# Kernel optimization log

Hardware: AMD Instinct MI355X
Metric: run time of the kernel (lower is better)

Reference implementation:

```python
import math
import jax, jax.numpy as jnp
import numpy as np

NEG_INF = -jnp.inf


def setup_inputs() -> dict:
    key = jax.random.key(0)
    k1, k2, k3 = jax.random.split(key, 3)
    B, T, D = 2, 2048, 1024
    x = jax.random.normal(k1, (B, T, D), dtype=jnp.float32)
    w_qkv = jax.random.normal(k2, (3 * D, D), dtype=jnp.float32) * (1.0 / math.sqrt(D))
    w_out = jax.random.normal(k3, (D, D), dtype=jnp.float32) * (1.0 / math.sqrt(D))
    return {"x": x, "w_qkv": w_qkv, "w_out": w_out, "n_heads": 16, "k": 8}


def reference(x, w_qkv, w_out, n_heads, k):
    B, T, D = x.shape
    head_dim = D // n_heads
    scale = math.sqrt(head_dim)

    qkv = x @ w_qkv.T                                   # (B,T,3D), torch Linear: x W^T
    q, kk, v = jnp.split(qkv, 3, axis=-1)

    def split_heads(t):
        return t.reshape(B, T, n_heads, head_dim).transpose(0, 2, 1, 3)  # (B,H,T,dh)

    q, kk, v = split_heads(q), split_heads(kk), split_heads(v)

    scores = jnp.einsum("bhqd,bhkd->bhqk", q, kk) / scale  # (B,H,T,T)
    causal = jnp.tril(jnp.ones((T, T), dtype=bool))
    scores = jnp.where(causal, scores, NEG_INF)

    # per-row effective k: min(k, n_valid) with n_valid = row index + 1
    top_vals = jax.lax.top_k(scores, k)[0]                 # (B,H,T,k), sorted desc
    k_eff_idx = jnp.minimum(jnp.arange(1, T + 1), k) - 1   # (T,)
    thresh = jnp.take_along_axis(
        top_vals, k_eff_idx[None, None, :, None], axis=-1  # (B,H,T,1)
    )
    keep = scores >= thresh                                # ties kept, matching torch >=
    scores = jnp.where(keep, scores, NEG_INF)

    attn = jax.nn.softmax(scores, axis=-1)
    attn = jnp.nan_to_num(attn)                            # defensive; rows never all -inf
    out = jnp.einsum("bhqk,bhkd->bhqd", attn, v)
    out = out.transpose(0, 2, 1, 3).reshape(B, T, D)       # merge heads
    return out @ w_out.T
```

## Files before the change

kernel.cpp:

```cpp
#include <hip/hip_runtime.h>
#include <hip/hip_bf16.h>
#include <math.h>
#include <float.h>

#define NUM_B 2
#define SEQ_T 2048
#define DIM_D 1024
#define NH 16
#define DH 64
#define KDIM 1024
#define KSEL 8

#define CAP 32
#define MFMA_MARGIN 0.06f

typedef __attribute__((ext_vector_type(8))) short bf16x8v;
typedef __attribute__((ext_vector_type(4))) float f32x4v;
typedef __attribute__((ext_vector_type(4))) double f64x4v;

__device__ __forceinline__ float bf2f(unsigned int u) {
  union { unsigned int i; float f; } v; v.i = u << 16; return v.f;
}

__device__ __forceinline__ short f2bs(float f) {
  __hip_bfloat16 h = __float2bfloat16(f);
  return *(short*)&h;
}

__device__ __forceinline__ void split8(float4 x0, float4 x1,
                                       unsigned short* __restrict__ hp,
                                       unsigned short* __restrict__ lp) {
  unsigned short h[8], l[8];
  const float xs[8] = {x0.x, x0.y, x0.z, x0.w, x1.x, x1.y, x1.z, x1.w};
#pragma unroll
  for (int j = 0; j < 8; ++j) {
    const short hb = f2bs(xs[j]);
    h[j] = (unsigned short)hb;
    const float hf = bf2f((unsigned int)(unsigned short)hb);
    l[j] = (unsigned short)f2bs(xs[j] - hf);
  }
  *(uint4*)hp = *(const uint4*)h;
  *(uint4*)lp = *(const uint4*)l;
}

__device__ __forceinline__ void split4(float4 x,
                                       unsigned short* __restrict__ hp,
                                       unsigned short* __restrict__ lp) {
  unsigned short h[4], l[4];
  const float xs[4] = {x.x, x.y, x.z, x.w};
#pragma unroll
  for (int j = 0; j < 4; ++j) {
    const short hb = f2bs(xs[j]);
    h[j] = (unsigned short)hb;
    const float hf = bf2f((unsigned int)(unsigned short)hb);
    l[j] = (unsigned short)f2bs(xs[j] - hf);
  }
  *(uint2*)hp = *(const uint2*)h;
  *(uint2*)lp = *(const uint2*)l;
}

__global__ __launch_bounds__(512) void gemm_qk(
    const float* __restrict__ A, const float* __restrict__ Bm,
    float* __restrict__ qbuf, float* __restrict__ kbuf,
    unsigned short* __restrict__ kbf) {
  __shared__ __align__(16) float As[64][36];
  __shared__ __align__(16) float Bs[128][36];
  const int tid = threadIdx.x;
  const int lane = tid & 63;
  const int w = tid >> 6;
  const int row0 = blockIdx.y * 64;
  const int col0 = blockIdx.x * 128;
  const int lrA = tid >> 3;
  const int lkA = (tid & 7) << 2;
  const int lrB = tid >> 2;
  const int lkB = (tid & 3) << 3;
  const float* ap = A + (size_t)(row0 + lrA) * KDIM + lkA;
  const float* bp = Bm + (size_t)(col0 + lrB) * KDIM + lkB;
  const int wr = (w >> 2) << 5;
  const int wc = (w & 3) << 5;
  const int li = lane & 15;
  const int lk4 = lane >> 4;

  int rowof[4], colof[4];
  {
    f64x4v pr = {0.0, 0.0, 0.0, 0.0};
    f64x4v pc = {0.0, 0.0, 0.0, 0.0};
    const double vidx = (double)li;
    pr = __builtin_amdgcn_mfma_f64_16x16x4f64(vidx, 1.0, pr, 0, 0, 0);
    pc = __builtin_amdgcn_mfma_f64_16x16x4f64(1.0, vidx, pc, 0, 0, 0);
#pragma unroll
    for (int vj = 0; vj < 4; ++vj) {
      rowof[vj] = (int)(pr[vj] * 0.25 + 0.5);
      colof[vj] = (int)(pc[vj] * 0.25 + 0.5);
    }
  }

  f64x4v acc[2][2];
#pragma unroll
  for (int m = 0; m < 2; ++m)
#pragma unroll
    for (int n = 0; n < 2; ++n)
      acc[m][n] = (f64x4v){0.0, 0.0, 0.0, 0.0};

  float4 ra = *(const float4*)(ap);
  float4 rb0 = *(const float4*)(bp);
  float4 rb1 = *(const float4*)(bp + 4);
  for (int k0 = 0; k0 < KDIM; k0 += 32) {
    __syncthreads();
    *(float4*)&As[lrA][lkA] = ra;
    *(float4*)&Bs[lrB][lkB] = rb0;
    *(float4*)&Bs[lrB][lkB + 4] = rb1;
    if (k0 + 32 < KDIM) {
      ra = *(const float4*)(ap + k0 + 32);
      rb0 = *(const float4*)(bp + k0 + 32);
      rb1 = *(const float4*)(bp + k0 + 36);
    }
    __syncthreads();
#pragma unroll
    for (int ks = 0; ks < 32; ks += 4) {
      const int kk = ks + lk4;
      const double af0 = (double)As[wr + li][kk];
      const double af1 = (double)As[wr + 16 + li][kk];
      const double bf0 = (double)Bs[wc + li][kk];
      const double bf1 = (double)Bs[wc + 16 + li][kk];
      acc[0][0] = __builtin_amdgcn_mfma_f64_16x16x4f64(af0, bf0, acc[0][0], 0, 0, 0);
      acc[0][1] = __builtin_amdgcn_mfma_f64_16x16x4f64(af0, bf1, acc[0][1], 0, 0, 0);
      acc[1][0] = __builtin_amdgcn_mfma_f64_16x16x4f64(af1, bf0, acc[1][0], 0, 0, 0);
      acc[1][1] = __builtin_amdgcn_mfma_f64_16x16x4f64(af1, bf1, acc[1][1], 0, 0, 0);
    }
  }

  const int bb = row0 >> 11;
  const int t0 = row0 & 2047;
#pragma unroll
  for (int m = 0; m < 2; ++m)
#pragma unroll
    for (int n = 0; n < 2; ++n)
#pragma unroll
      for (int vj = 0; vj < 4; ++vj) {
        const int r = wr + 16 * m + rowof[vj];
        const int gc = col0 + wc + 16 * n + colof[vj];
        const int qi = gc >> 10;
        const int head = (gc & 1023) >> 6;
        const int d = gc & 63;
        const int t = t0 + r;
        const float fv = (float)acc[m][n][vj];
        float* dst = ((qi == 0) ? qbuf : kbuf) +
                     (size_t)(bb * NH + head) * SEQ_T * DH;
        dst[(size_t)t * DH + d] = fv;
        if (qi == 1) {
          unsigned short* kb = kbf + ((size_t)(bb * NH + head) << 17);
          const int key = t & 127;
          const int off =
              (((t >> 7) << 13) | (key << 6) | d) ^ ((key & 7) << 3);
          __hip_bfloat16 hb = __float2bfloat16(fv);
          kb[off] = *(unsigned short*)&hb;
        }
      }
}

__global__ __launch_bounds__(512) void gemm_v(
    const float* __restrict__ A, const float* __restrict__ Bm,
    unsigned short* __restrict__ vbuf) {
  __shared__ __align__(16) unsigned short Ah[64][40];
  __shared__ __align__(16) unsigned short Al[64][40];
  __shared__ __align__(16) unsigned short Bh[128][40];
  __shared__ __align__(16) unsigned short Bl[128][40];
  const int tid = threadIdx.x;
  const int lane = tid & 63;
  const int w = tid >> 6;
  const int row0 = blockIdx.y * 64;
  const int col0v = blockIdx.x * 128;
  const int lrA = tid >> 3;
  const int lkA = (tid & 7) << 2;
  const int lrB = tid >> 2;
  const int lkB = (tid & 3) << 3;
  const float* ap = A + (size_t)(row0 + lrA) * KDIM + lkA;
  const float* bp = Bm + (size_t)(col0v + lrB) * KDIM + lkB;
  const int wr = (w >> 2) << 5;
  const int wc = (w & 3) << 5;
  const int li = lane & 15;
  const int kA = (lane >> 4) << 3;

  f32x4v acc[2][2];
#pragma unroll
  for (int m = 0; m < 2; ++m)
#pragma unroll
    for (int n = 0; n < 2; ++n)
      acc[m][n] = (f32x4v){0.f, 0.f, 0.f, 0.f};

  float4 ra = *(const float4*)(ap);
  float4 rb0 = *(const float4*)(bp);
  float4 rb1 = *(const float4*)(bp + 4);
  for (int k0 = 0; k0 < KDIM; k0 += 32) {
    __syncthreads();
    split4(ra, &Ah[lrA][lkA], &Al[lrA][lkA]);
    split8(rb0, rb1, &Bh[lrB][lkB], &Bl[lrB][lkB]);
    if (k0 + 32 < KDIM) {
      ra = *(const float4*)(ap + k0 + 32);
      rb0 = *(const float4*)(bp + k0 + 32);
      rb1 = *(const float4*)(bp + k0 + 36);
    }
    __syncthreads();
    bf16x8v ah[2], al[2], bh[2], bl[2];
#pragma unroll
    for (int m = 0; m < 2; ++m) {
      ah[m] = *(const bf16x8v*)&Ah[wr + 16 * m + li][kA];
      al[m] = *(const bf16x8v*)&Al[wr + 16 * m + li][kA];
      bh[m] = *(const bf16x8v*)&Bh[wc + 16 * m + li][kA];
      bl[m] = *(const bf16x8v*)&Bl[wc + 16 * m + li][kA];
    }
#pragma unroll
    for (int m = 0; m < 2; ++m)
#pragma unroll
      for (int n = 0; n < 2; ++n) {
        acc[m][n] = __builtin_amdgcn_mfma_f32_16x16x32_bf16(ah[m], bh[n], acc[m][n], 0, 0, 0);
        acc[m][n] = __builtin_amdgcn_mfma_f32_16x16x32_bf16(ah[m], bl[n], acc[m][n], 0, 0, 0);
        acc[m][n] = __builtin_amdgcn_mfma_f32_16x16x32_bf16(al[m], bh[n], acc[m][n], 0, 0, 0);
      }
  }

  const int bb = row0 >> 11;
  const int t0 = row0 & 2047;
  const int r4 = (lane >> 4) << 2;
#pragma unroll
  for (int m = 0; m < 2; ++m)
#pragma unroll
    for (int n = 0; n < 2; ++n)
#pragma unroll
      for (int j = 0; j < 4; ++j) {
        const int t = t0 + wr + 16 * m + r4 + j;
        const int vcol = col0v + wc + 16 * n + li;
        const int head = vcol >> 6;
        const int d = vcol & 63;
        vbuf[(size_t)(bb * NH + head) * SEQ_T * DH + (size_t)t * DH + d] =
            (unsigned short)f2bs(acc[m][n][j]);
      }
}

__global__ __launch_bounds__(512) void attn_topk(
    const float* __restrict__ q, const float* __restrict__ kmat,
    const unsigned short* __restrict__ kbf,
    const unsigned short* __restrict__ v, unsigned short* __restrict__ ctx) {
  __shared__ __align__(16) unsigned short kt[128 * 64];
  __shared__ double cs64[128][CAP];
  __shared__ short ckey[128][CAP];
  __shared__ int ccnt[128];
  __shared__ double rthr[128];
  __shared__ float rmx[128];

  const int tid = threadIdx.x;
  const int lane = tid & 63;
  const int w = tid >> 6;
  const int bh = blockIdx.x & 31;
  const int u = blockIdx.x >> 5;
  const int g = (u < 8) ? u : 23 - u;
  const int t0 = g << 7;
  const size_t kbase = (size_t)bh * SEQ_T * DH;
  const int wrow0 = t0 + (w << 4);
  const int kA = (lane >> 4) << 3;
  const int rbase = wrow0 + ((lane >> 4) << 2);

  bf16x8v qa0, qa1;
  {
    const float* qr = q + kbase + (size_t)(wrow0 + (lane & 15)) * DH;
    const float4 x0 = *(const float4*)(qr + kA);
    const float4 x1 = *(const float4*)(qr + kA + 4);
    const float4 y0 = *(const float4*)(qr + 32 + kA);
    const float4 y1 = *(const float4*)(qr + 32 + kA + 4);
    qa0[0] = f2bs(x0.x); qa0[1] = f2bs(x0.y);
    qa0[2] = f2bs(x0.z); qa0[3] = f2bs(x0.w);
    qa0[4] = f2bs(x1.x); qa0[5] = f2bs(x1.y);
    qa0[6] = f2bs(x1.z); qa0[7] = f2bs(x1.w);
    qa1[0] = f2bs(y0.x); qa1[1] = f2bs(y0.y);
    qa1[2] = f2bs(y0.z); qa1[3] = f2bs(y0.w);
    qa1[4] = f2bs(y1.x); qa1[5] = f2bs(y1.y);
    qa1[6] = f2bs(y1.z); qa1[7] = f2bs(y1.w);
  }

  const uint4* ksrc = (const uint4*)(kbf + ((size_t)bh << 17));
  const int nt = (t0 >> 7) + 1;
  const int wmax = wrow0 + 15;

  float tq[4][8];
#pragma unroll
  for (int j = 0; j < 4; ++j)
#pragma unroll
    for (int m = 0; m < 8; ++m) tq[j][m] = -FLT_MAX;

  for (int T = 0; T < nt; ++T) {
    if (T) __syncthreads();
    {
      const uint4* st = ksrc + (size_t)T * 1024;
      uint4* dv = (uint4*)kt;
#pragma unroll
      for (int i = 0; i < 2; ++i) dv[i * 512 + tid] = st[i * 512 + tid];
    }
    __syncthreads();
    const int glim0 = (wmax - (T << 7)) >> 4;
    const int glim = glim0 > 7 ? 7 : glim0;
    for (int gt = 0; gt <= glim; ++gt) {
      const int kk = (gt << 4) + (lane & 15);
      const int key = (T << 7) + kk;
      const int b0 = ((kk << 7) | (kA << 1)) ^ ((kk & 7) << 4);
      const int b1 = ((kk << 7) | ((32 + kA) << 1)) ^ ((kk & 7) << 4);
      const bf16x8v kb0 = *(const bf16x8v*)((const char*)kt + b0);
      const bf16x8v kb1 = *(const bf16x8v*)((const char*)kt + b1);
      f32x4v acc = {0.f, 0.f, 0.f, 0.f};
      acc = __builtin_amdgcn_mfma_f32_16x16x32_bf16(qa0, kb0, acc, 0, 0, 0);
      acc = __builtin_amdgcn_mfma_f32_16x16x32_bf16(qa1, kb1, acc, 0, 0, 0);
#pragma unroll
      for (int j = 0; j < 4; ++j) {
        float sc = acc[j] * 0.125f;
        sc = (key <= rbase + j) ? sc : -FLT_MAX;
        if (sc > tq[j][7]) {
          float s = sc;
#pragma unroll
          for (int m = 0; m < 8; ++m) {
            const float hi = fmaxf(tq[j][m], s);
            s = fminf(tq[j][m], s);
            tq[j][m] = hi;
          }
        }
      }
    }
  }

#pragma unroll
  for (int j = 0; j < 4; ++j) {
#pragma unroll
    for (int xm = 1; xm < 16; xm <<= 1) {
      float m[8];
#pragma unroll
      for (int i = 0; i < 8; ++i) {
        const float pb = __shfl_xor(tq[j][7 - i], xm);
        m[i] = fmaxf(tq[j][i], pb);
      }
#pragma unroll
      for (int d = 4; d >= 1; d >>= 1)
#pragma unroll
        for (int i = 0; i < 8; ++i)
          if ((i & d) == 0 && (i | d) < 8) {
            const float hi = fmaxf(m[i], m[i | d]);
            const float lo = fminf(m[i], m[i | d]);
            m[i] = hi;
            m[i | d] = lo;
          }
#pragma unroll
      for (int i = 0; i < 8; ++i) tq[j][i] = m[i];
    }
  }
  float thrj[4];
#pragma unroll
  for (int j = 0; j < 4; ++j) {
    const int kf = (rbase + j + 1 < KSEL) ? (rbase + j + 1) : KSEL;
    float th = tq[j][7];
#pragma unroll
    for (int m = 0; m < 8; ++m)
      if (m == kf - 1) th = tq[j][m];
    thrj[j] = th - MFMA_MARGIN;
  }

  if (tid < 128) ccnt[tid] = 0;
  __syncthreads();

  for (int T = 0; T < nt; ++T) {
    if (T) __syncthreads();
    {
      const uint4* st = ksrc + (size_t)T * 1024;
      uint4* dv = (uint4*)kt;
#pragma unroll
      for (int i = 0; i < 2; ++i) dv[i * 512 + tid] = st[i * 512 + tid];
    }
    __syncthreads();
    const int glim0 = (wmax - (T << 7)) >> 4;
    const int glim = glim0 > 7 ? 7 : glim0;
    for (int gt = 0; gt <= glim; ++gt) {
      const int kk = (gt << 4) + (lane & 15);
      const int key = (T << 7) + kk;
      const int b0 = ((kk << 7) | (kA << 1)) ^ ((kk & 7) << 4);
      const int b1 = ((kk << 7) | ((32 + kA) << 1)) ^ ((kk & 7) << 4);
      const bf16x8v kb0 = *(const bf16x8v*)((const char*)kt + b0);
      const bf16x8v kb1 = *(const bf16x8v*)((const char*)kt + b1);
      f32x4v acc = {0.f, 0.f, 0.f, 0.f};
      acc = __builtin_amdgcn_mfma_f32_16x16x32_bf16(qa0, kb0, acc, 0, 0, 0);
      acc = __builtin_amdgcn_mfma_f32_16x16x32_bf16(qa1, kb1, acc, 0, 0, 0);
#pragma unroll
      for (int j = 0; j < 4; ++j) {
        const float sc = acc[j] * 0.125f;
        if (key <= rbase + j && sc >= thrj[j]) {
          const int rl = (w << 4) + ((lane >> 4) << 2) + j;
          const int p = atomicAdd(&ccnt[rl], 1);
          if (p < CAP) ckey[rl][p] = (short)key;
        }
      }
    }
  }

  const int lid = lane & 31;
  for (int rp = 0; rp < 8; ++rp) {
    const int rl = (w << 4) + (rp << 1) + (lane >> 5);
    const int ncc = ccnt[rl] < CAP ? ccnt[rl] : CAP;
    if (lid < ncc) {
      const int key = ckey[rl][lid];
      const float* qr = q + kbase + (size_t)(t0 + rl) * DH;
      const float* kr = kmat + kbase + (size_t)key * DH;
      double s = 0.0;
#pragma unroll
      for (int d4 = 0; d4 < 16; ++d4) {
        const float4 qq = *(const float4*)(qr + (d4 << 2));
        const float4 kq = *(const float4*)(kr + (d4 << 2));
        s = fma((double)qq.x, (double)kq.x, s);
        s = fma((double)qq.y, (double)kq.y, s);
        s = fma((double)qq.z, (double)kq.z, s);
        s = fma((double)qq.w, (double)kq.w, s);
      }
      cs64[rl][lid] = s * 0.125;
    }
  }
  __syncthreads();

  if (lane < 16) {
    const int rl = (w << 4) + lane;
    const int trow = t0 + rl;
    const int ncc = ccnt[rl] < CAP ? ccnt[rl] : CAP;
    double a64[8];
#pragma unroll
    for (int j = 0; j < 8; ++j) a64[j] = -DBL_MAX;
    for (int l = 0; l < ncc; ++l) {
      double sv = cs64[rl][l];
#pragma unroll
      for (int j = 0; j < 8; ++j) {
        const double hi = fmax(a64[j], sv);
        sv = fmin(a64[j], sv);
        a64[j] = hi;
      }
    }
    const int kf = (trow + 1 < KSEL) ? (trow + 1) : KSEL;
    double th = a64[7];
#pragma unroll
    for (int j = 0; j < 8; ++j)
      if (j == kf - 1) th = a64[j];
    rthr[rl] = th;
    rmx[rl] = (float)a64[0];
  }
  __syncthreads();

  for (int rg = 0; rg < 4; ++rg) {
    const int rlb = (w << 4) + (rg << 2);
    float acv[4] = {0.f, 0.f, 0.f, 0.f};
    float Zs[4] = {0.f, 0.f, 0.f, 0.f};
    int ncs[4];
    double ths[4];
    float mxs[4];
#pragma unroll
    for (int j = 0; j < 4; ++j) {
      const int rl = rlb + j;
      ncs[j] = ccnt[rl] < CAP ? ccnt[rl] : CAP;
      ths[j] = rthr[rl];
      mxs[j] = rmx[rl];
    }
    int nmax = ncs[0];
#pragma unroll
    for (int j = 1; j < 4; ++j) nmax = ncs[j] > nmax ? ncs[j] : nmax;
    for (int l = 0; l < nmax; ++l) {
#pragma unroll
      for (int j = 0; j < 4; ++j) {
        const int rl = rlb + j;
        if (l < ncs[j]) {
          const double s = cs64[rl][l];
          const float wgl = (s >= ths[j]) ? expf((float)s - mxs[j]) : 0.f;
          Zs[j] += wgl;
          acv[j] = fmaf(
              wgl,
              bf2f((unsigned int)v[kbase + (size_t)ckey[rl][l] * DH + lane]),
              acv[j]);
        }
      }
    }
#pragma unroll
    for (int j = 0; j < 4; ++j) {
      const int trow = t0 + rlb + j;
      __hip_bfloat16 h = __float2bfloat16(acv[j] / Zs[j]);
      ctx[((size_t)(bh >> 4) * SEQ_T + trow) * DIM_D + (bh & 15) * DH + lane] =
          *(unsigned short*)&h;
    }
  }
}

__global__ __launch_bounds__(256) void gemm_out(
    const unsigned short* __restrict__ A, const float* __restrict__ Bm,
    float* __restrict__ obuf) {
  __shared__ __align__(16) unsigned short Ah[64][40];
  __shared__ __align__(16) unsigned short Bh[64][40];
  __shared__ __align__(16) unsigned short Bl[64][40];
  const int tid = threadIdx.x;
  const int lane = tid & 63;
  const int w = tid >> 6;
  const int row0 = blockIdx.y * 64;
  const int col0 = blockIdx.x * 64;
  const int lrow = tid >> 2;
  const int lk = (tid & 3) << 3;
  const unsigned short* ap = A + (size_t)(row0 + lrow) * KDIM + lk;
  const float* bp = Bm + (size_t)(col0 + lrow) * KDIM + lk;
  const int wr = (w >> 1) << 5;
  const int wc = (w & 1) << 5;
  const int li = lane & 15;
  const int kA = (lane >> 4) << 3;

  f32x4v acc[2][2];
#pragma unroll
  for (int m = 0; m < 2; ++m)
#pragma unroll
    for (int n = 0; n < 2; ++n)
      acc[m][n] = (f32x4v){0.f, 0.f, 0.f, 0.f};

  uint4 ua = *(const uint4*)(ap);
  float4 rb0 = *(const float4*)(bp);
  float4 rb1 = *(const float4*)(bp + 4);
  for (int k0 = 0; k0 < KDIM; k0 += 32) {
    __syncthreads();
    *(uint4*)&Ah[lrow][lk] = ua;
    split8(rb0, rb1, &Bh[lrow][lk], &Bl[lrow][lk]);
    if (k0 + 32 < KDIM) {
      ua = *(const uint4*)(ap + k0 + 32);
      rb0 = *(const float4*)(bp + k0 + 32);
      rb1 = *(const float4*)(bp + k0 + 36);
    }
    __syncthreads();
    bf16x8v ah[2], bh[2], bl[2];
#pragma unroll
    for (int m = 0; m < 2; ++m) {
      ah[m] = *(const bf16x8v*)&Ah[wr + 16 * m + li][kA];
      bh[m] = *(const bf16x8v*)&Bh[wc + 16 * m + li][kA];
      bl[m] = *(const bf16x8v*)&Bl[wc + 16 * m + li][kA];
    }
#pragma unroll
    for (int m = 0; m < 2; ++m)
#pragma unroll
      for (int n = 0; n < 2; ++n) {
        acc[m][n] = __builtin_amdgcn_mfma_f32_16x16x32_bf16(ah[m], bh[n], acc[m][n], 0, 0, 0);
        acc[m][n] = __builtin_amdgcn_mfma_f32_16x16x32_bf16(ah[m], bl[n], acc[m][n], 0, 0, 0);
      }
  }

  const int r4 = (lane >> 4) << 2;
#pragma unroll
  for (int m = 0; m < 2; ++m)
#pragma unroll
    for (int n = 0; n < 2; ++n)
#pragma unroll
      for (int j = 0; j < 4; ++j) {
        const int r = row0 + wr + 16 * m + r4 + j;
        const int c = col0 + wc + 16 * n + li;
        obuf[(size_t)r * DIM_D + c] = acc[m][n][j];
      }
}

extern "C" void kernel_launch(void* const* d_in, const int* in_sizes, int n_in,
                              void* d_out, int out_size, void* d_ws,
                              size_t ws_size, hipStream_t stream) {
  (void)out_size; (void)ws_size;
  const float* x = (const float*)d_in[0];
  const float* wqkv = (const float*)d_in[1];
  const float* wout = (const float*)d_in[2];
  for (int i = 0; i < n_in; ++i) {
    if (in_sizes[i] == NUM_B * SEQ_T * DIM_D) x = (const float*)d_in[i];
    else if (in_sizes[i] == 3 * DIM_D * DIM_D) wqkv = (const float*)d_in[i];
    else if (in_sizes[i] == DIM_D * DIM_D) wout = (const float*)d_in[i];
  }
  float* out = (float*)d_out;

  const size_t qkv_elems = (size_t)NUM_B * NH * SEQ_T * DH;
  float* qbuf = (float*)d_ws;
  float* kbuf = qbuf + qkv_elems;
  unsigned short* vbuf = (unsigned short*)(kbuf + qkv_elems);
  unsigned short* ctxb = vbuf + qkv_elems;
  unsigned short* kbf = ctxb + (size_t)NUM_B * SEQ_T * DIM_D;

  gemm_qk<<<dim3(2 * DIM_D / 128, NUM_B * SEQ_T / 64), 512, 0, stream>>>(
      x, wqkv, qbuf, kbuf, kbf);
  gemm_v<<<dim3(DIM_D / 128, NUM_B * SEQ_T / 64), 512, 0, stream>>>(
      x, wqkv + (size_t)2 * DIM_D * KDIM, vbuf);
  attn_topk<<<dim3(NUM_B * NH * (SEQ_T / 128)), 512, 0, stream>>>(
      qbuf, kbuf, kbf, vbuf, ctxb);
  gemm_out<<<dim3(DIM_D / 64, NUM_B * SEQ_T / 64), 256, 0, stream>>>(
      ctxb, wout, out);
}
```

Before: 599.4 us.

## Split top-k attention into scan and selection kernels via global candidate buffer

The fused attention kernel is split in two. A scan kernel runs the MFMA score pass and writes per-row candidate keys and counts to workspace. A second kernel with 256 threads and 64-row tiles rescoring candidates in double precision, then does softmax and the V product. Moving the large double-precision shared arrays out of the scan kernel should cut its LDS footprint and raise occupancy, and the selection stage gets a finer grid. The cost is an extra launch plus a global round trip for the candidate lists, and the workspace layout must fit the new buffers.

```diff
diff --git a/kernel.cpp b/kernel.cpp
--- a/kernel.cpp
+++ b/kernel.cpp
@@ -238,16 +238,12 @@
       }
 }
 
-__global__ __launch_bounds__(512) void attn_topk(
-    const float* __restrict__ q, const float* __restrict__ kmat,
-    const unsigned short* __restrict__ kbf,
-    const unsigned short* __restrict__ v, unsigned short* __restrict__ ctx) {
+__global__ __launch_bounds__(512) void attn_scan(
+    const float* __restrict__ q, const unsigned short* __restrict__ kbf,
+    short* __restrict__ gckey, int* __restrict__ gccnt) {
   __shared__ __align__(16) unsigned short kt[128 * 64];
-  __shared__ double cs64[128][CAP];
-  __shared__ short ckey[128][CAP];
+  __shared__ __align__(16) short ckey[128][CAP];
   __shared__ int ccnt[128];
-  __shared__ double rthr[128];
-  __shared__ float rmx[128];
 
   const int tid = threadIdx.x;
   const int lane = tid & 63;
@@ -396,6 +392,42 @@
       }
     }
   }
+
+  __syncthreads();
+  {
+    const int row = tid >> 2;
+    const int sl = (tid & 3) << 3;
+    *(uint4*)&gckey[((size_t)bh * SEQ_T + t0 + row) * CAP + sl] =
+        *(const uint4*)&ckey[row][sl];
+    if (tid < 128) gccnt[(size_t)bh * SEQ_T + t0 + tid] = ccnt[tid];
+  }
+}
+
+__global__ __launch_bounds__(256) void attn_sel(
+    const float* __restrict__ q, const float* __restrict__ kmat,
+    const short* __restrict__ gckey, const int* __restrict__ gccnt,
+    const unsigned short* __restrict__ v, unsigned short* __restrict__ ctx) {
+  __shared__ __align__(16) double cs64[64][CAP];
+  __shared__ __align__(16) short ckey[64][CAP];
+  __shared__ int ccnt[64];
+  __shared__ double rthr[64];
+  __shared__ float rmx[64];
+
+  const int tid = threadIdx.x;
+  const int lane = tid & 63;
+  const int w = tid >> 6;
+  const int bh = blockIdx.x & 31;
+  const int t0 = (blockIdx.x >> 5) << 6;
+  const size_t kbase = (size_t)bh * SEQ_T * DH;
+
+  {
+    const int row = tid >> 2;
+    const int sl = (tid & 3) << 3;
+    *(uint4*)&ckey[row][sl] =
+        *(const uint4*)&gckey[((size_t)bh * SEQ_T + t0 + row) * CAP + sl];
+    if (tid < 64) ccnt[tid] = gccnt[(size_t)bh * SEQ_T + t0 + tid];
+  }
+  __syncthreads();
 
   const int lid = lane & 31;
   for (int rp = 0; rp < 8; ++rp) {
@@ -577,13 +609,17 @@
   unsigned short* vbuf = (unsigned short*)(kbuf + qkv_elems);
   unsigned short* ctxb = vbuf + qkv_elems;
   unsigned short* kbf = ctxb + (size_t)NUM_B * SEQ_T * DIM_D;
+  short* gckey = (short*)(kbf + ((size_t)NUM_B * NH << 17));
+  int* gccnt = (int*)(gckey + (size_t)NUM_B * NH * SEQ_T * CAP);
 
   gemm_qk<<<dim3(2 * DIM_D / 128, NUM_B * SEQ_T / 64), 512, 0, stream>>>(
       x, wqkv, qbuf, kbuf, kbf);
   gemm_v<<<dim3(DIM_D / 128, NUM_B * SEQ_T / 64), 512, 0, stream>>>(
       x, wqkv + (size_t)2 * DIM_D * KDIM, vbuf);
-  attn_topk<<<dim3(NUM_B * NH * (SEQ_T / 128)), 512, 0, stream>>>(
-      qbuf, kbuf, kbf, vbuf, ctxb);
+  attn_scan<<<dim3(NUM_B * NH * (SEQ_T / 128)), 512, 0, stream>>>(
+      qbuf, kbf, gckey, gccnt);
+  attn_sel<<<dim3(NUM_B * NH * (SEQ_T / 64)), 256, 0, stream>>>(
+      qbuf, kbuf, gckey, gccnt, vbuf, ctxb);
   gemm_out<<<dim3(DIM_D / 64, NUM_B * SEQ_T / 64), 256, 0, stream>>>(
       ctxb, wout, out);
 }
```

Measured after the change: 613.7 us. 1.02x slower.
